# Kernel optimization log

Measured on AMD Instinct MI355X. Metric: run time of the kernel, lower is better.

Reference implementation:

```python
import jax, jax.numpy as jnp
import numpy as np

EPS = 1e-05


def layer_norm(x, a, b):
    m = jnp.mean(x, axis=-1, keepdims=True)
    v = jnp.var(x, axis=-1, keepdims=True)
    return a * (x - m) / jnp.sqrt(v + EPS) + b


def setup_inputs() -> dict:
    key = jax.random.key(0)
    ks = jax.random.split(key, 16)
    b, n, d, h = 1, 384, 128, 128
    s = 1.0 / np.sqrt(d)
    inp = {
        "x": jax.random.normal(ks[0], (b, n, n, d), dtype=jnp.float32),
        "norm_a": jnp.ones((d,), jnp.float32),
        "norm_b": jnp.zeros((d,), jnp.float32),
        "Wl": jax.random.normal(ks[1], (d, h), jnp.float32) * s,
        "bl": jnp.zeros((h,), jnp.float32),
        "Wr": jax.random.normal(ks[2], (d, h), jnp.float32) * s,
        "br": jnp.zeros((h,), jnp.float32),
        "Wlg": jax.random.normal(ks[3], (d, h), jnp.float32) * s,
        "blg": jnp.ones((h,), jnp.float32),
        "Wrg": jax.random.normal(ks[4], (d, h), jnp.float32) * s,
        "brg": jnp.ones((h,), jnp.float32),
        "Wog": jax.random.normal(ks[5], (d, h), jnp.float32) * s,
        "bog": jnp.ones((h,), jnp.float32),
        "on_a": jnp.ones((h,), jnp.float32),
        "on_b": jnp.zeros((h,), jnp.float32),
        "Wo": jax.random.normal(ks[6], (h, d), jnp.float32) * s,
        "bo": jnp.zeros((d,), jnp.float32),
    }
    return inp


def reference(x, norm_a, norm_b, Wl, bl, Wr, br, Wlg, blg, Wrg, brg, Wog, bog, on_a, on_b, Wo, bo):
    n = x.shape[1]
    xn = layer_norm(x, norm_a, norm_b)
    left = (xn @ Wl + bl) * jax.nn.sigmoid(xn @ Wlg + blg)
    right = (xn @ Wr + br) * jax.nn.sigmoid(xn @ Wrg + brg)
    out_gate = jax.nn.sigmoid(xn @ Wog + bog)
    # ingoing mix: out[b,i,j,d] = sum_k left[b,k,j,d] * right[b,k,i,d], in fp32
    out = jnp.einsum('bkjd,bkid->bijd', left.astype(jnp.float32), right.astype(jnp.float32)) / n
    out = out.astype(x.dtype)
    out = layer_norm(out, on_a, on_b) * out_gate
    return out @ Wo + bo
```

## Files before the change

kernel.cpp:

```cpp
#include <hip/hip_runtime.h>
#include <hip/hip_bf16.h>

#define NN 384
#define DD 128
#define MM (NN*NN)

typedef __attribute__((ext_vector_type(8))) short short8;
typedef __attribute__((ext_vector_type(4))) float f32x4;

__device__ __forceinline__ unsigned short f2bf(float f){
  unsigned u = __float_as_uint(f);
  u += 0x7fffu + ((u >> 16) & 1u);
  return (unsigned short)(u >> 16);
}
__device__ __forceinline__ float bf2f(unsigned short u){
  return __uint_as_float(((unsigned)u) << 16);
}
__device__ __forceinline__ float sigm(float x){
  return 1.0f / (1.0f + __expf(-x));
}
__device__ __forceinline__ unsigned cvtpk(float lo, float hi){
  unsigned r;
  asm("v_cvt_pk_bf16_f32 %0, %1, %2" : "=v"(r) : "v"(lo), "v"(hi));
  return r;
}
__device__ __forceinline__ f32x4 mfma16(short8 a, short8 b, f32x4 c){
  return __builtin_amdgcn_mfma_f32_16x16x32_bf16(a, b, c, 0, 0, 0);
}
__device__ __forceinline__ void gll16(const void* g, void* l){
  __builtin_amdgcn_global_load_lds(
      (const __attribute__((address_space(1))) unsigned int*)g,
      (__attribute__((address_space(3))) unsigned int*)l, 16, 0, 0);
}

__global__ void k_prep(const float* __restrict__ Wl, const float* __restrict__ Wlg,
                       const float* __restrict__ Wr, const float* __restrict__ Wrg,
                       const float* __restrict__ Wog, const float* __restrict__ Wo,
                       unsigned short* __restrict__ Wcat, unsigned short* __restrict__ Wot){
  int n = blockIdx.x;
  if(n < 640){
    const float* src; int col;
    if(n < 128){ src = Wl;  col = n; }
    else if(n < 256){ src = Wlg; col = n-128; }
    else if(n < 384){ src = Wr;  col = n-256; }
    else if(n < 512){ src = Wrg; col = n-384; }
    else            { src = Wog; col = n-512; }
    for(int k = threadIdx.x; k < 128; k += 64)
      Wcat[n*128 + k] = f2bf(src[k*128 + col]);
  } else {
    int c = n - 640;
    for(int k = threadIdx.x; k < 128; k += 64)
      Wot[c*128 + k] = f2bf(Wo[k*128 + c]);
  }
}

__global__ __launch_bounds__(256) void k_ln_x(const float* __restrict__ x,
    const float* __restrict__ na, const float* __restrict__ nb,
    unsigned short* __restrict__ xn){
  int wid = threadIdx.x >> 6, lane = threadIdx.x & 63;
  long r = (long)blockIdx.x*4 + wid;
  float2 v = *(const float2*)(x + r*DD + lane*2);
  float s  = v.x + v.y;
  float sq = v.x*v.x + v.y*v.y;
  #pragma unroll
  for(int m = 32; m >= 1; m >>= 1){ s += __shfl_xor(s, m); sq += __shfl_xor(sq, m); }
  float mean = s  * (1.0f/128.0f);
  float var  = sq * (1.0f/128.0f) - mean*mean;
  float rstd = rsqrtf(var + 1e-5f);
  float2 a = *(const float2*)(na + lane*2);
  float2 b = *(const float2*)(nb + lane*2);
  unsigned pk = (unsigned)f2bf(a.x*(v.x-mean)*rstd + b.x)
              | ((unsigned)f2bf(a.y*(v.y-mean)*rstd + b.y) << 16);
  *(unsigned*)(xn + r*DD + lane*2) = pk;
}

__global__ __launch_bounds__(256, 4) void k_proj(
    const unsigned short* __restrict__ xn, const unsigned short* __restrict__ Wcat,
    const float* __restrict__ bl, const float* __restrict__ blg,
    const float* __restrict__ br, const float* __restrict__ brg,
    unsigned short* __restrict__ Lt, unsigned short* __restrict__ Rt){
  __shared__ char lds[2][16384];
  const int tid = threadIdx.x;
  const int wid = tid >> 6, lane = tid & 63;
  const int lrow = lane & 15, lgrp = lane >> 4;
  const int b = blockIdx.x;
  const int f = b / 288;
  const int w = b % 288;

  const int ws = wid >> 1;
  const int wd = wid & 1;
  const int d  = f*32 + wd*16 + lrow;

  short8 bv[4], bg[4];
  #pragma unroll
  for(int ks = 0; ks < 4; ++ks){
    bv[ks] = *(const short8*)(Wcat + (ws*256 + d)*DD + ks*32 + lgrp*8);
    bg[ks] = *(const short8*)(Wcat + (ws*256 + 128 + d)*DD + ks*32 + lgrp*8);
  }
  const float b0v = (ws ? br  : bl )[d];
  const float b1v = (ws ? brg : blg)[d];
  const float sc  = ws ? 1.0f : (1.0f/384.0f);
  unsigned short* const base = (ws ? Rt : Lt) + (long)d*MM;

  auto stage = [&](int buf, int v){
    int j = v/6, kb = v%6;
    int rsub = lane >> 4, c = lane & 15;
    #pragma unroll
    for(int p = 0; p < 4; ++p){
      int r0 = p*16 + wid*4;
      int r = r0 + rsub;
      gll16(xn + ((long)(kb*64 + r)*NN + j)*DD + (c ^ (r & 7))*8, &lds[buf][r0*256]);
    }
  };

  stage(0, w*8);
  __syncthreads();
  int cur = 0;
  for(int i = 0; i < 8; ++i){
    int v = w*8 + i;
    if(i < 7) stage(cur^1, v+1);

    f32x4 zero = {0.f,0.f,0.f,0.f};
    f32x4 acc[4][2];
    #pragma unroll
    for(int a1=0;a1<4;++a1){ acc[a1][0] = zero; acc[a1][1] = zero; }

    #pragma unroll
    for(int ks = 0; ks < 4; ++ks){
      #pragma unroll
      for(int fr = 0; fr < 4; ++fr){
        int r = fr*16 + lrow;
        short8 af = *(const short8*)(&lds[cur][r*256 + (((ks*4+lgrp)*16) ^ ((r&7)<<4))]);
        acc[fr][0] = mfma16(af, bv[ks], acc[fr][0]);
        acc[fr][1] = mfma16(af, bg[ks], acc[fr][1]);
      }
    }

    int j = v/6, kb = v%6;
    unsigned short* dst = base + (long)j*NN + kb*64;
    #pragma unroll
    for(int fr = 0; fr < 4; ++fr){
      float v0 = (acc[fr][0][0] + b0v)*sigm(acc[fr][1][0] + b1v)*sc;
      float v1 = (acc[fr][0][1] + b0v)*sigm(acc[fr][1][1] + b1v)*sc;
      float v2 = (acc[fr][0][2] + b0v)*sigm(acc[fr][1][2] + b1v)*sc;
      float v3 = (acc[fr][0][3] + b0v)*sigm(acc[fr][1][3] + b1v)*sc;
      uint2 pk; pk.x = cvtpk(v0, v1); pk.y = cvtpk(v2, v3);
      *(uint2*)(dst + fr*16 + lgrp*4) = pk;
    }
    __syncthreads();
    cur ^= 1;
  }
}

__global__ __launch_bounds__(256) void k_einsum(
    const unsigned short* __restrict__ Rt, const unsigned short* __restrict__ Lt,
    unsigned short* __restrict__ mid){
  __shared__ char lds[65536];
  const int b = blockIdx.x;
  const int xcd = b & 7, slot = b >> 3;
  const int d = (slot/9)*8 + xcd;
  const int t = slot % 9;
  const int it = t/3, jt = t%3;
  const int i0 = it*128, j0 = jt*128;
  const unsigned short* Abase = Lt + (long)d*MM;
  const unsigned short* Bbase = Rt + (long)d*MM;
  const int wid = threadIdx.x >> 6, lane = threadIdx.x & 63;
  const int wr = wid >> 1, wc = wid & 1;
  const int lrow = lane & 15, lgrp = lane >> 4;

  auto stage = [&](int buf, int kt){
    int k = kt*64;
    int c = lane & 7;
    #pragma unroll
    for(int t8 = 0; t8 < 8; ++t8){
      int rr = wid*64 + t8*8 + (lane >> 3);
      int r = rr & 127;
      const unsigned short* src = (rr < 128) ? (Abase + (long)(j0+r)*NN + k)
                                             : (Bbase + (long)(i0+r)*NN + k);
      gll16(src + (c ^ (r & 7))*8, &lds[buf*32768 + (wid*64 + t8*8)*128]);
    }
  };

  f32x4 zero = {0.f,0.f,0.f,0.f};
  f32x4 acc[4][4];
  #pragma unroll
  for(int a1 = 0; a1 < 4; ++a1)
    #pragma unroll
    for(int a2 = 0; a2 < 4; ++a2) acc[a1][a2] = zero;

  stage(0, 0);
  __syncthreads();
  for(int kt = 0; kt < 6; ++kt){
    int cur = kt & 1;
    if(kt < 5) stage(cur ^ 1, kt + 1);
    const int base = cur*32768;
    #pragma unroll
    for(int ks = 0; ks < 2; ++ks){
      short8 af[4], bf[4];
      #pragma unroll
      for(int f = 0; f < 4; ++f){
        int rj = wr*64 + f*16 + lrow;
        af[f] = *(const short8*)(&lds[base + rj*128 + (((ks*4+lgrp)*16) ^ ((rj & 7) << 4))]);
        int ri = wc*64 + f*16 + lrow;
        bf[f] = *(const short8*)(&lds[base + 16384 + ri*128 + (((ks*4+lgrp)*16) ^ ((ri & 7) << 4))]);
      }
      #pragma unroll
      for(int fj = 0; fj < 4; ++fj)
        #pragma unroll
        for(int fi = 0; fi < 4; ++fi)
          acc[fj][fi] = mfma16(af[fj], bf[fi], acc[fj][fi]);
    }
    __syncthreads();
  }

  #pragma unroll
  for(int fj = 0; fj < 4; ++fj){
    int j = j0 + wr*64 + fj*16 + lgrp*4;
    #pragma unroll
    for(int fi = 0; fi < 4; ++fi){
      int i = i0 + wc*64 + fi*16 + lrow;
      uint2 pk;
      pk.x = cvtpk(acc[fj][fi][0], acc[fj][fi][1]);
      pk.y = cvtpk(acc[fj][fi][2], acc[fj][fi][3]);
      *(uint2*)(mid + (long)d*MM + (long)i*NN + j) = pk;
    }
  }
}

__global__ __launch_bounds__(256) void k_final(
    const unsigned short* __restrict__ mid, const unsigned short* __restrict__ xn,
    const unsigned short* __restrict__ Wcat,
    const float* __restrict__ bog,
    const float* __restrict__ ona, const float* __restrict__ onb,
    const unsigned short* __restrict__ Wot, const float* __restrict__ bo,
    float* __restrict__ out){
  __shared__ unsigned short midt[64][144];
  __shared__ char slds[16384];
  __shared__ char glds[16384];
  const int tid = threadIdx.x;
  const int wid = tid >> 6, lane = tid & 63;
  const int lrow = lane & 15, lgrp = lane >> 4;
  const int i = blockIdx.y;
  const int j0 = blockIdx.x*64;

  {
    int rsub = lane >> 4, c = lane & 15;
    #pragma unroll
    for(int p = 0; p < 4; ++p){
      int r0 = p*16 + wid*4;
      int r = r0 + rsub;
      gll16(xn + ((long)i*NN + j0 + r)*DD + (c ^ (r & 7))*8, &slds[r0*256]);
    }
  }
  const int wc = wid;
  short8 ag[2][4];
  #pragma unroll
  for(int cf = 0; cf < 2; ++cf)
    #pragma unroll
    for(int ks = 0; ks < 4; ++ks)
      ag[cf][ks] = *(const short8*)(Wcat + (512 + wc*32 + cf*16 + lrow)*DD + ks*32 + lgrp*8);

  {
    int jp = tid & 15, dr = tid >> 4;
    #pragma unroll
    for(int pass = 0; pass < 8; ++pass){
      int dd = pass*16 + dr;
      uint2 v = *(const uint2*)(mid + (long)dd*MM + (long)i*NN + j0 + jp*4);
      midt[jp*4+0][dd] = (unsigned short)(v.x & 0xffffu);
      midt[jp*4+1][dd] = (unsigned short)(v.x >> 16);
      midt[jp*4+2][dd] = (unsigned short)(v.y & 0xffffu);
      midt[jp*4+3][dd] = (unsigned short)(v.y >> 16);
    }
  }
  __syncthreads();

  {
    f32x4 zero = {0.f,0.f,0.f,0.f};
    f32x4 accg[2][4];
    #pragma unroll
    for(int a1=0;a1<2;++a1)
      #pragma unroll
      for(int a2=0;a2<4;++a2) accg[a1][a2] = zero;
    #pragma unroll
    for(int ks = 0; ks < 4; ++ks){
      short8 bx[4];
      #pragma unroll
      for(int mf = 0; mf < 4; ++mf){
        int r = mf*16 + lrow;
        bx[mf] = *(const short8*)(&slds[r*256 + (((ks*4+lgrp)*16) ^ ((r&7)<<4))]);
      }
      #pragma unroll
      for(int cf = 0; cf < 2; ++cf)
        #pragma unroll
        for(int mf = 0; mf < 4; ++mf)
          accg[cf][mf] = mfma16(ag[cf][ks], bx[mf], accg[cf][mf]);
    }
    #pragma unroll
    for(int cf = 0; cf < 2; ++cf){
      int c0 = wc*32 + cf*16 + lgrp*4;
      float4 b4 = *(const float4*)(bog + c0);
      #pragma unroll
      for(int mf = 0; mf < 4; ++mf){
        int rr = mf*16 + lrow;
        uint2 pk;
        pk.x = cvtpk(sigm(accg[cf][mf][0] + b4.x), sigm(accg[cf][mf][1] + b4.y));
        pk.y = cvtpk(sigm(accg[cf][mf][2] + b4.z), sigm(accg[cf][mf][3] + b4.w));
        *(uint2*)(&glds[rr*256 + ((c0*2) ^ ((rr&7)<<4))]) = pk;
      }
    }
  }
  __syncthreads();

  {
    int j = tid >> 2, s = tid & 3;
    float vals[32];
    float sum = 0.f, sq = 0.f;
    #pragma unroll
    for(int o8 = 0; o8 < 4; ++o8){
      short8 h = *(const short8*)(&midt[j][s*32 + o8*8]);
      #pragma unroll
      for(int q = 0; q < 8; ++q){
        float vq = bf2f((unsigned short)h[q]);
        vals[o8*8+q] = vq; sum += vq; sq += vq*vq;
      }
    }
    #pragma unroll
    for(int m = 1; m < 4; m <<= 1){ sum += __shfl_xor(sum, m); sq += __shfl_xor(sq, m); }
    float mean = sum*(1.f/128.f);
    float var  = sq *(1.f/128.f) - mean*mean;
    float rstd = rsqrtf(var + 1e-5f);
    #pragma unroll
    for(int o = 0; o < 32; o += 4){
      int dd = s*32 + o;
      uint2 gv = *(const uint2*)(&glds[j*256 + ((dd*2) ^ ((j&7)<<4))]);
      float g0 = bf2f((unsigned short)(gv.x & 0xffffu));
      float g1 = bf2f((unsigned short)(gv.x >> 16));
      float g2 = bf2f((unsigned short)(gv.y & 0xffffu));
      float g3 = bf2f((unsigned short)(gv.y >> 16));
      float4 a4 = *(const float4*)(ona + dd);
      float4 b4 = *(const float4*)(onb + dd);
      float v0 = (a4.x*(vals[o]  -mean)*rstd + b4.x)*g0;
      float v1 = (a4.y*(vals[o+1]-mean)*rstd + b4.y)*g1;
      float v2 = (a4.z*(vals[o+2]-mean)*rstd + b4.z)*g2;
      float v3 = (a4.w*(vals[o+3]-mean)*rstd + b4.w)*g3;
      uint2 pk; pk.x = cvtpk(v0, v1); pk.y = cvtpk(v2, v3);
      *(uint2*)(&slds[j*256 + ((dd*2) ^ ((j&7)<<4))]) = pk;
    }
  }
  __syncthreads();

  {
    f32x4 zero = {0.f,0.f,0.f,0.f};
    f32x4 acc[8];
    #pragma unroll
    for(int fc = 0; fc < 8; ++fc) acc[fc] = zero;
    #pragma unroll 1
    for(int ks = 0; ks < 4; ++ks){
      int row = wid*16 + lrow;
      short8 a = *(const short8*)(&slds[row*256 + (((ks*4+lgrp)*16) ^ ((row & 7) << 4))]);
      #pragma unroll
      for(int fc = 0; fc < 8; ++fc){
        int n = fc*16 + lrow;
        short8 bfr = *(const short8*)(Wot + n*DD + ks*32 + lgrp*8);
        acc[fc] = mfma16(a, bfr, acc[fc]);
      }
    }
    #pragma unroll
    for(int fc = 0; fc < 8; ++fc){
      int c = fc*16 + lrow;
      float bb = bo[c];
      #pragma unroll
      for(int q = 0; q < 4; ++q){
        int jl = wid*16 + lgrp*4 + q;
        out[((long)i*NN + j0 + jl)*DD + c] = acc[fc][q] + bb;
      }
    }
  }
}

extern "C" void kernel_launch(void* const* d_in, const int* in_sizes, int n_in,
                              void* d_out, int out_size, void* d_ws, size_t ws_size,
                              hipStream_t stream){
  const float* x   = (const float*)d_in[0];
  const float* na  = (const float*)d_in[1];
  const float* nb  = (const float*)d_in[2];
  const float* Wl  = (const float*)d_in[3];
  const float* bl  = (const float*)d_in[4];
  const float* Wr  = (const float*)d_in[5];
  const float* br  = (const float*)d_in[6];
  const float* Wlg = (const float*)d_in[7];
  const float* blg = (const float*)d_in[8];
  const float* Wrg = (const float*)d_in[9];
  const float* brg = (const float*)d_in[10];
  const float* Wog = (const float*)d_in[11];
  const float* bog = (const float*)d_in[12];
  const float* ona = (const float*)d_in[13];
  const float* onb = (const float*)d_in[14];
  const float* Wo  = (const float*)d_in[15];
  const float* bo  = (const float*)d_in[16];
  float* out = (float*)d_out;

  char* ws = (char*)d_ws;
  const size_t SZ = (size_t)MM*DD*2;
  unsigned short* xn   = (unsigned short*)(ws);
  unsigned short* Lt   = (unsigned short*)(ws + SZ);
  unsigned short* Rt   = (unsigned short*)(ws + 2*SZ);
  unsigned short* mid  = (unsigned short*)(ws + 3*SZ);
  unsigned short* Wcat = (unsigned short*)(ws + 4*SZ);
  unsigned short* Wot  = (unsigned short*)(ws + 4*SZ + (size_t)640*128*2);

  k_prep  <<<768, 64, 0, stream>>>(Wl, Wlg, Wr, Wrg, Wog, Wo, Wcat, Wot);
  k_ln_x  <<<MM/4, 256, 0, stream>>>(x, na, nb, xn);
  k_proj  <<<1152, 256, 0, stream>>>(xn, Wcat, bl, blg, br, brg, Lt, Rt);
  k_einsum<<<1152, 256, 0, stream>>>(Rt, Lt, mid);
  k_final <<<dim3(6, 384), 256, 0, stream>>>(mid, xn, Wcat, bog, ona, onb, Wot, bo, out);
}
```

Measured before the change: 197.2 us.

## Reuse one LDS buffer for gate and output, preload Wo fragments, vectorize stores

```diff
diff --git a/kernel.cpp b/kernel.cpp
--- a/kernel.cpp
+++ b/kernel.cpp
@@ -234,14 +234,14 @@
     const float* __restrict__ ona, const float* __restrict__ onb,
     const unsigned short* __restrict__ Wot, const float* __restrict__ bo,
     float* __restrict__ out){
-  __shared__ unsigned short midt[64][144];
+  __shared__ unsigned short midt[64][136];
   __shared__ char slds[16384];
-  __shared__ char glds[16384];
   const int tid = threadIdx.x;
   const int wid = tid >> 6, lane = tid & 63;
   const int lrow = lane & 15, lgrp = lane >> 4;
   const int i = blockIdx.y;
   const int j0 = blockIdx.x*64;
+  const int wc = wid;
 
   {
     int rsub = lane >> 4, c = lane & 15;
@@ -252,7 +252,6 @@
       gll16(xn + ((long)i*NN + j0 + r)*DD + (c ^ (r & 7))*8, &slds[r0*256]);
     }
   }
-  const int wc = wid;
   short8 ag[2][4];
   #pragma unroll
   for(int cf = 0; cf < 2; ++cf)
@@ -274,27 +273,37 @@
   }
   __syncthreads();
 
+  f32x4 zero = {0.f,0.f,0.f,0.f};
+  f32x4 accg[2][4];
+  #pragma unroll
+  for(int a1=0;a1<2;++a1)
+    #pragma unroll
+    for(int a2=0;a2<4;++a2) accg[a1][a2] = zero;
+  #pragma unroll
+  for(int ks = 0; ks < 4; ++ks){
+    short8 bx[4];
+    #pragma unroll
+    for(int mf = 0; mf < 4; ++mf){
+      int r = mf*16 + lrow;
+      bx[mf] = *(const short8*)(&slds[r*256 + (((ks*4+lgrp)*16) ^ ((r&7)<<4))]);
+    }
+    #pragma unroll
+    for(int cf = 0; cf < 2; ++cf)
+      #pragma unroll
+      for(int mf = 0; mf < 4; ++mf)
+        accg[cf][mf] = mfma16(ag[cf][ks], bx[mf], accg[cf][mf]);
+  }
+
+  short8 aw[2][4];
+  #pragma unroll
+  for(int cf = 0; cf < 2; ++cf)
+    #pragma unroll
+    for(int ks = 0; ks < 4; ++ks)
+      aw[cf][ks] = *(const short8*)(Wot + (wc*32 + cf*16 + lrow)*DD + ks*32 + lgrp*8);
+
+  __syncthreads();
+
   {
-    f32x4 zero = {0.f,0.f,0.f,0.f};
-    f32x4 accg[2][4];
-    #pragma unroll
-    for(int a1=0;a1<2;++a1)
-      #pragma unroll
-      for(int a2=0;a2<4;++a2) accg[a1][a2] = zero;
-    #pragma unroll
-    for(int ks = 0; ks < 4; ++ks){
-      short8 bx[4];
-      #pragma unroll
-      for(int mf = 0; mf < 4; ++mf){
-        int r = mf*16 + lrow;
-        bx[mf] = *(const short8*)(&slds[r*256 + (((ks*4+lgrp)*16) ^ ((r&7)<<4))]);
-      }
-      #pragma unroll
-      for(int cf = 0; cf < 2; ++cf)
-        #pragma unroll
-        for(int mf = 0; mf < 4; ++mf)
-          accg[cf][mf] = mfma16(ag[cf][ks], bx[mf], accg[cf][mf]);
-    }
     #pragma unroll
     for(int cf = 0; cf < 2; ++cf){
       int c0 = wc*32 + cf*16 + lgrp*4;
@@ -305,7 +314,7 @@
         uint2 pk;
         pk.x = cvtpk(sigm(accg[cf][mf][0] + b4.x), sigm(accg[cf][mf][1] + b4.y));
         pk.y = cvtpk(sigm(accg[cf][mf][2] + b4.z), sigm(accg[cf][mf][3] + b4.w));
-        *(uint2*)(&glds[rr*256 + ((c0*2) ^ ((rr&7)<<4))]) = pk;
+        *(uint2*)(&slds[rr*256 + ((c0*2) ^ ((rr&7)<<4))]) = pk;
       }
     }
   }
@@ -332,7 +341,8 @@
     #pragma unroll
     for(int o = 0; o < 32; o += 4){
       int dd = s*32 + o;
-      uint2 gv = *(const uint2*)(&glds[j*256 + ((dd*2) ^ ((j&7)<<4))]);
+      char* gp = &slds[j*256 + ((dd*2) ^ ((j&7)<<4))];
+      uint2 gv = *(uint2*)gp;
       float g0 = bf2f((unsigned short)(gv.x & 0xffffu));
       float g1 = bf2f((unsigned short)(gv.x >> 16));
       float g2 = bf2f((unsigned short)(gv.y & 0xffffu));
@@ -344,35 +354,44 @@
       float v2 = (a4.z*(vals[o+2]-mean)*rstd + b4.z)*g2;
       float v3 = (a4.w*(vals[o+3]-mean)*rstd + b4.w)*g3;
       uint2 pk; pk.x = cvtpk(v0, v1); pk.y = cvtpk(v2, v3);
-      *(uint2*)(&slds[j*256 + ((dd*2) ^ ((j&7)<<4))]) = pk;
+      *(uint2*)gp = pk;
     }
   }
   __syncthreads();
 
   {
-    f32x4 zero = {0.f,0.f,0.f,0.f};
-    f32x4 acc[8];
-    #pragma unroll
-    for(int fc = 0; fc < 8; ++fc) acc[fc] = zero;
-    #pragma unroll 1
+    f32x4 acco[2][4];
+    #pragma unroll
+    for(int a1=0;a1<2;++a1)
+      #pragma unroll
+      for(int a2=0;a2<4;++a2) acco[a1][a2] = zero;
+    #pragma unroll
     for(int ks = 0; ks < 4; ++ks){
-      int row = wid*16 + lrow;
-      short8 a = *(const short8*)(&slds[row*256 + (((ks*4+lgrp)*16) ^ ((row & 7) << 4))]);
-      #pragma unroll
-      for(int fc = 0; fc < 8; ++fc){
-        int n = fc*16 + lrow;
-        short8 bfr = *(const short8*)(Wot + n*DD + ks*32 + lgrp*8);
-        acc[fc] = mfma16(a, bfr, acc[fc]);
-      }
-    }
-    #pragma unroll
-    for(int fc = 0; fc < 8; ++fc){
-      int c = fc*16 + lrow;
-      float bb = bo[c];
-      #pragma unroll
-      for(int q = 0; q < 4; ++q){
-        int jl = wid*16 + lgrp*4 + q;
-        out[((long)i*NN + j0 + jl)*DD + c] = acc[fc][q] + bb;
+      short8 bx[4];
+      #pragma unroll
+      for(int mf = 0; mf < 4; ++mf){
+        int r = mf*16 + lrow;
+        bx[mf] = *(const short8*)(&slds[r*256 + (((ks*4+lgrp)*16) ^ ((r&7)<<4))]);
+      }
+      #pragma unroll
+      for(int cf = 0; cf < 2; ++cf)
+        #pragma unroll
+        for(int mf = 0; mf < 4; ++mf)
+          acco[cf][mf] = mfma16(aw[cf][ks], bx[mf], acco[cf][mf]);
+    }
+    #pragma unroll
+    for(int cf = 0; cf < 2; ++cf){
+      int c0 = wc*32 + cf*16 + lgrp*4;
+      float4 b4 = *(const float4*)(bo + c0);
+      #pragma unroll
+      for(int mf = 0; mf < 4; ++mf){
+        int jl = mf*16 + lrow;
+        float4 v;
+        v.x = acco[cf][mf][0] + b4.x;
+        v.y = acco[cf][mf][1] + b4.y;
+        v.z = acco[cf][mf][2] + b4.z;
+        v.w = acco[cf][mf][3] + b4.w;
+        *(float4*)(out + ((long)i*NN + j0 + jl)*DD + c0) = v;
       }
     }
   }
```

New measurement: 180.1 us. -8.6%, faster.

## Make final kernel persistent over three tiles with double-buffered xn and mid prefetch

Applied to the files above, without the earlier changes.

```diff
diff --git a/kernel.cpp b/kernel.cpp
--- a/kernel.cpp
+++ b/kernel.cpp
@@ -227,155 +227,193 @@
   }
 }
 
-__global__ __launch_bounds__(256) void k_final(
+__global__ __launch_bounds__(256, 3) void k_final(
     const unsigned short* __restrict__ mid, const unsigned short* __restrict__ xn,
     const unsigned short* __restrict__ Wcat,
     const float* __restrict__ bog,
     const float* __restrict__ ona, const float* __restrict__ onb,
     const unsigned short* __restrict__ Wot, const float* __restrict__ bo,
     float* __restrict__ out){
-  __shared__ unsigned short midt[64][144];
-  __shared__ char slds[16384];
-  __shared__ char glds[16384];
+  __shared__ char Xb[2][16384];
+  __shared__ unsigned short midt[64][136];
+  __shared__ float clds[512];
   const int tid = threadIdx.x;
   const int wid = tid >> 6, lane = tid & 63;
   const int lrow = lane & 15, lgrp = lane >> 4;
-  const int i = blockIdx.y;
-  const int j0 = blockIdx.x*64;
-
-  {
-    int rsub = lane >> 4, c = lane & 15;
-    #pragma unroll
-    for(int p = 0; p < 4; ++p){
-      int r0 = p*16 + wid*4;
-      int r = r0 + rsub;
-      gll16(xn + ((long)i*NN + j0 + r)*DD + (c ^ (r & 7))*8, &slds[r0*256]);
-    }
-  }
-  const int wc = wid;
-  short8 ag[2][4];
+  const int jp = tid & 15, dr = tid >> 4;
+  const int u0 = blockIdx.x * 3;
+
+  uint2 mA[8], mB[8];
+
+#define STAGE_XN(buf, uu) {                                                   \
+    int i_ = (uu)/6, jj_ = ((uu)%6)*64;                                       \
+    int rsub = lane >> 4, cc = lane & 15;                                     \
+    _Pragma("unroll")                                                         \
+    for(int p = 0; p < 4; ++p){                                               \
+      int r0 = p*16 + wid*4;                                                  \
+      int r = r0 + rsub;                                                      \
+      gll16(xn + ((long)i_*NN + jj_ + r)*DD + (cc ^ (r & 7))*8,               \
+            &Xb[buf][r0*256]);                                                \
+    } }
+
+#define LOAD_MID(reg, uu) {                                                   \
+    int i_ = (uu)/6, jj_ = ((uu)%6)*64;                                       \
+    const unsigned short* mp = mid + (long)i_*NN + jj_ + jp*4;                \
+    _Pragma("unroll")                                                         \
+    for(int p = 0; p < 8; ++p)                                                \
+      reg[p] = *(const uint2*)(mp + (long)(p*16 + dr)*MM);                    \
+  }
+
+#define WRITE_MIDT(reg) {                                                     \
+    _Pragma("unroll")                                                         \
+    for(int p = 0; p < 8; ++p){                                               \
+      int dd = p*16 + dr;                                                     \
+      midt[jp*4+0][dd] = (unsigned short)(reg[p].x & 0xffffu);                \
+      midt[jp*4+1][dd] = (unsigned short)(reg[p].x >> 16);                    \
+      midt[jp*4+2][dd] = (unsigned short)(reg[p].y & 0xffffu);                \
+      midt[jp*4+3][dd] = (unsigned short)(reg[p].y >> 16);                    \
+    } }
+
+  short8 ag[2][4], aw[2][4];
   #pragma unroll
   for(int cf = 0; cf < 2; ++cf)
     #pragma unroll
-    for(int ks = 0; ks < 4; ++ks)
-      ag[cf][ks] = *(const short8*)(Wcat + (512 + wc*32 + cf*16 + lrow)*DD + ks*32 + lgrp*8);
-
-  {
-    int jp = tid & 15, dr = tid >> 4;
-    #pragma unroll
-    for(int pass = 0; pass < 8; ++pass){
-      int dd = pass*16 + dr;
-      uint2 v = *(const uint2*)(mid + (long)dd*MM + (long)i*NN + j0 + jp*4);
-      midt[jp*4+0][dd] = (unsigned short)(v.x & 0xffffu);
-      midt[jp*4+1][dd] = (unsigned short)(v.x >> 16);
-      midt[jp*4+2][dd] = (unsigned short)(v.y & 0xffffu);
-      midt[jp*4+3][dd] = (unsigned short)(v.y >> 16);
-    }
-  }
+    for(int ks = 0; ks < 4; ++ks){
+      ag[cf][ks] = *(const short8*)(Wcat + (512 + wid*32 + cf*16 + lrow)*DD + ks*32 + lgrp*8);
+      aw[cf][ks] = *(const short8*)(Wot  + (      wid*32 + cf*16 + lrow)*DD + ks*32 + lgrp*8);
+    }
+  if(tid < 128){
+    clds[tid]       = ona[tid];
+    clds[128 + tid] = onb[tid];
+    clds[256 + tid] = bog[tid];
+    clds[384 + tid] = bo[tid];
+  }
+
+  STAGE_XN(0, u0);
+  LOAD_MID(mA, u0);
   __syncthreads();
 
-  {
-    f32x4 zero = {0.f,0.f,0.f,0.f};
-    f32x4 accg[2][4];
-    #pragma unroll
-    for(int a1=0;a1<2;++a1)
-      #pragma unroll
-      for(int a2=0;a2<4;++a2) accg[a1][a2] = zero;
-    #pragma unroll
-    for(int ks = 0; ks < 4; ++ks){
-      short8 bx[4];
-      #pragma unroll
-      for(int mf = 0; mf < 4; ++mf){
-        int r = mf*16 + lrow;
-        bx[mf] = *(const short8*)(&slds[r*256 + (((ks*4+lgrp)*16) ^ ((r&7)<<4))]);
-      }
-      #pragma unroll
-      for(int cf = 0; cf < 2; ++cf)
-        #pragma unroll
-        for(int mf = 0; mf < 4; ++mf)
-          accg[cf][mf] = mfma16(ag[cf][ks], bx[mf], accg[cf][mf]);
-    }
-    #pragma unroll
-    for(int cf = 0; cf < 2; ++cf){
-      int c0 = wc*32 + cf*16 + lgrp*4;
-      float4 b4 = *(const float4*)(bog + c0);
-      #pragma unroll
-      for(int mf = 0; mf < 4; ++mf){
-        int rr = mf*16 + lrow;
-        uint2 pk;
-        pk.x = cvtpk(sigm(accg[cf][mf][0] + b4.x), sigm(accg[cf][mf][1] + b4.y));
-        pk.y = cvtpk(sigm(accg[cf][mf][2] + b4.z), sigm(accg[cf][mf][3] + b4.w));
-        *(uint2*)(&glds[rr*256 + ((c0*2) ^ ((rr&7)<<4))]) = pk;
-      }
-    }
-  }
-  __syncthreads();
-
-  {
-    int j = tid >> 2, s = tid & 3;
-    float vals[32];
-    float sum = 0.f, sq = 0.f;
-    #pragma unroll
-    for(int o8 = 0; o8 < 4; ++o8){
-      short8 h = *(const short8*)(&midt[j][s*32 + o8*8]);
-      #pragma unroll
-      for(int q = 0; q < 8; ++q){
-        float vq = bf2f((unsigned short)h[q]);
-        vals[o8*8+q] = vq; sum += vq; sq += vq*vq;
-      }
-    }
-    #pragma unroll
-    for(int m = 1; m < 4; m <<= 1){ sum += __shfl_xor(sum, m); sq += __shfl_xor(sq, m); }
-    float mean = sum*(1.f/128.f);
-    float var  = sq *(1.f/128.f) - mean*mean;
-    float rstd = rsqrtf(var + 1e-5f);
-    #pragma unroll
-    for(int o = 0; o < 32; o += 4){
-      int dd = s*32 + o;
-      uint2 gv = *(const uint2*)(&glds[j*256 + ((dd*2) ^ ((j&7)<<4))]);
-      float g0 = bf2f((unsigned short)(gv.x & 0xffffu));
-      float g1 = bf2f((unsigned short)(gv.x >> 16));
-      float g2 = bf2f((unsigned short)(gv.y & 0xffffu));
-      float g3 = bf2f((unsigned short)(gv.y >> 16));
-      float4 a4 = *(const float4*)(ona + dd);
-      float4 b4 = *(const float4*)(onb + dd);
-      float v0 = (a4.x*(vals[o]  -mean)*rstd + b4.x)*g0;
-      float v1 = (a4.y*(vals[o+1]-mean)*rstd + b4.y)*g1;
-      float v2 = (a4.z*(vals[o+2]-mean)*rstd + b4.z)*g2;
-      float v3 = (a4.w*(vals[o+3]-mean)*rstd + b4.w)*g3;
-      uint2 pk; pk.x = cvtpk(v0, v1); pk.y = cvtpk(v2, v3);
-      *(uint2*)(&slds[j*256 + ((dd*2) ^ ((j&7)<<4))]) = pk;
-    }
-  }
-  __syncthreads();
-
-  {
-    f32x4 zero = {0.f,0.f,0.f,0.f};
-    f32x4 acc[8];
-    #pragma unroll
-    for(int fc = 0; fc < 8; ++fc) acc[fc] = zero;
-    #pragma unroll 1
-    for(int ks = 0; ks < 4; ++ks){
-      int row = wid*16 + lrow;
-      short8 a = *(const short8*)(&slds[row*256 + (((ks*4+lgrp)*16) ^ ((row & 7) << 4))]);
-      #pragma unroll
-      for(int fc = 0; fc < 8; ++fc){
-        int n = fc*16 + lrow;
-        short8 bfr = *(const short8*)(Wot + n*DD + ks*32 + lgrp*8);
-        acc[fc] = mfma16(a, bfr, acc[fc]);
-      }
-    }
-    #pragma unroll
-    for(int fc = 0; fc < 8; ++fc){
-      int c = fc*16 + lrow;
-      float bb = bo[c];
-      #pragma unroll
-      for(int q = 0; q < 4; ++q){
-        int jl = wid*16 + lgrp*4 + q;
-        out[((long)i*NN + j0 + jl)*DD + c] = acc[fc][q] + bb;
-      }
-    }
-  }
+#define UNIT(T, MREG, MNXT, CUR) {                                            \
+    const int u_ = u0 + (T);                                                  \
+    const int iU = u_/6, jU = (u_%6)*64;                                      \
+    if((T) < 2){ STAGE_XN((CUR)^1, u_+1); LOAD_MID(MNXT, u_+1); }             \
+    WRITE_MIDT(MREG);                                                         \
+    f32x4 zero_ = {0.f,0.f,0.f,0.f};                                          \
+    f32x4 accg[2][4];                                                         \
+    _Pragma("unroll")                                                         \
+    for(int a1=0;a1<2;++a1){ _Pragma("unroll")                                \
+      for(int a2=0;a2<4;++a2) accg[a1][a2] = zero_; }                         \
+    _Pragma("unroll")                                                         \
+    for(int ks = 0; ks < 4; ++ks){                                            \
+      short8 bx[4];                                                           \
+      _Pragma("unroll")                                                       \
+      for(int mf = 0; mf < 4; ++mf){                                          \
+        int r = mf*16 + lrow;                                                 \
+        bx[mf] = *(const short8*)(&Xb[CUR][r*256 + (((ks*4+lgrp)*16) ^ ((r&7)<<4))]); \
+      }                                                                       \
+      _Pragma("unroll")                                                       \
+      for(int cf = 0; cf < 2; ++cf){ _Pragma("unroll")                        \
+        for(int mf = 0; mf < 4; ++mf)                                         \
+          accg[cf][mf] = mfma16(ag[cf][ks], bx[mf], accg[cf][mf]); }          \
+    }                                                                         \
+    __syncthreads();   \
+    _Pragma("unroll")                                                         \
+    for(int cf = 0; cf < 2; ++cf){                                            \
+      int c0 = wid*32 + cf*16 + lgrp*4;                                       \
+      float4 g4 = *(const float4*)&clds[256 + c0];                            \
+      _Pragma("unroll")                                                       \
+      for(int mf = 0; mf < 4; ++mf){                                          \
+        int rr = mf*16 + lrow;                                                \
+        uint2 pk;                                                             \
+        pk.x = cvtpk(sigm(accg[cf][mf][0]+g4.x), sigm(accg[cf][mf][1]+g4.y)); \
+        pk.y = cvtpk(sigm(accg[cf][mf][2]+g4.z), sigm(accg[cf][mf][3]+g4.w)); \
+        *(uint2*)(&Xb[CUR][rr*256 + ((c0*2) ^ ((rr&7)<<4))]) = pk;            \
+      }                                                                       \
+    }                                                                         \
+    __syncthreads();                                      \
+    {                                                                         \
+      int j_ = tid >> 2, s_ = tid & 3;                                        \
+      float sum = 0.f, sq = 0.f;                                              \
+      _Pragma("unroll")                                                       \
+      for(int o8 = 0; o8 < 4; ++o8){                                          \
+        short8 h = *(const short8*)(&midt[j_][s_*32 + o8*8]);                 \
+        _Pragma("unroll")                                                     \
+        for(int q = 0; q < 8; ++q){                                           \
+          float vq = bf2f((unsigned short)h[q]);                              \
+          sum += vq; sq += vq*vq;                                             \
+        }                                                                     \
+      }                                                                       \
+      sum += __shfl_xor(sum,1); sq += __shfl_xor(sq,1);                       \
+      sum += __shfl_xor(sum,2); sq += __shfl_xor(sq,2);                       \
+      float mean = sum*(1.f/128.f);                                           \
+      float var  = sq *(1.f/128.f) - mean*mean;                               \
+      float rstd = rsqrtf(var + 1e-5f);                                       \
+      _Pragma("unroll")                                                       \
+      for(int o = 0; o < 32; o += 4){                                         \
+        int dd = s_*32 + o;                                                   \
+        char* gp = &Xb[CUR][j_*256 + ((dd*2) ^ ((j_&7)<<4))];                 \
+        uint2 gv = *(uint2*)gp;                                               \
+        uint2 mv = *(const uint2*)(&midt[j_][dd]);                            \
+        float m0 = bf2f((unsigned short)(mv.x & 0xffffu));                    \
+        float m1 = bf2f((unsigned short)(mv.x >> 16));                        \
+        float m2 = bf2f((unsigned short)(mv.y & 0xffffu));                    \
+        float m3 = bf2f((unsigned short)(mv.y >> 16));                        \
+        float4 a4 = *(const float4*)&clds[dd];                                \
+        float4 b4 = *(const float4*)&clds[128 + dd];                          \
+        float v0 = (a4.x*(m0-mean)*rstd + b4.x)*bf2f((unsigned short)(gv.x & 0xffffu)); \
+        float v1 = (a4.y*(m1-mean)*rstd + b4.y)*bf2f((unsigned short)(gv.x >> 16));     \
+        float v2 = (a4.z*(m2-mean)*rstd + b4.z)*bf2f((unsigned short)(gv.y & 0xffffu)); \
+        float v3 = (a4.w*(m3-mean)*rstd + b4.w)*bf2f((unsigned short)(gv.y >> 16));     \
+        uint2 pk; pk.x = cvtpk(v0, v1); pk.y = cvtpk(v2, v3);                 \
+        *(uint2*)gp = pk;                                                     \
+      }                                                                       \
+    }                                                                         \
+    __syncthreads();                                       \
+    {                                                                         \
+      f32x4 acco[2][4];                                                       \
+      _Pragma("unroll")                                                       \
+      for(int a1=0;a1<2;++a1){ _Pragma("unroll")                              \
+        for(int a2=0;a2<4;++a2) acco[a1][a2] = zero_; }                       \
+      _Pragma("unroll")                                                       \
+      for(int ks = 0; ks < 4; ++ks){                                          \
+        short8 bx[4];                                                         \
+        _Pragma("unroll")                                                     \
+        for(int mf = 0; mf < 4; ++mf){                                        \
+          int r = mf*16 + lrow;                                               \
+          bx[mf] = *(const short8*)(&Xb[CUR][r*256 + (((ks*4+lgrp)*16) ^ ((r&7)<<4))]); \
+        }                                                                     \
+        _Pragma("unroll")                                                     \
+        for(int cf = 0; cf < 2; ++cf){ _Pragma("unroll")                      \
+          for(int mf = 0; mf < 4; ++mf)                                       \
+            acco[cf][mf] = mfma16(aw[cf][ks], bx[mf], acco[cf][mf]); }        \
+      }                                                                       \
+      _Pragma("unroll")                                                       \
+      for(int cf = 0; cf < 2; ++cf){                                          \
+        int c0 = wid*32 + cf*16 + lgrp*4;                                     \
+        float4 b4 = *(const float4*)&clds[384 + c0];                          \
+        _Pragma("unroll")                                                     \
+        for(int mf = 0; mf < 4; ++mf){                                        \
+          int jl = mf*16 + lrow;                                              \
+          float4 v;                                                           \
+          v.x = acco[cf][mf][0] + b4.x;                                       \
+          v.y = acco[cf][mf][1] + b4.y;                                       \
+          v.z = acco[cf][mf][2] + b4.z;                                       \
+          v.w = acco[cf][mf][3] + b4.w;                                       \
+          *(float4*)(out + ((long)iU*NN + jU + jl)*DD + c0) = v;              \
+        }                                                                     \
+      }                                                                       \
+    }                                                                         \
+    __syncthreads();  \
+  }
+
+  UNIT(0, mA, mB, 0)
+  UNIT(1, mB, mA, 1)
+  UNIT(2, mA, mB, 0)
+
+#undef UNIT
+#undef STAGE_XN
+#undef LOAD_MID
+#undef WRITE_MIDT
 }
 
 extern "C" void kernel_launch(void* const* d_in, const int* in_sizes, int n_in,
@@ -413,5 +451,5 @@
   k_ln_x  <<<MM/4, 256, 0, stream>>>(x, na, nb, xn);
   k_proj  <<<1152, 256, 0, stream>>>(xn, Wcat, bl, blg, br, brg, Lt, Rt);
   k_einsum<<<1152, 256, 0, stream>>>(Rt, Lt, mid);
-  k_final <<<dim3(6, 384), 256, 0, stream>>>(mid, xn, Wcat, bog, ona, onb, Wot, bo, out);
-}
+  k_final <<<768, 256, 0, stream>>>(mid, xn, Wcat, bog, ona, onb, Wot, bo, out);
+}
```

Measured after the change: 166.7 us. 15.4% less time.

## Restructure final kernel: two tiles per block with register prefetch and reduced LDS

Applied to the files above, without the earlier changes.

```diff
diff --git a/kernel.cpp b/kernel.cpp
--- a/kernel.cpp
+++ b/kernel.cpp
@@ -31,6 +31,10 @@
   __builtin_amdgcn_global_load_lds(
       (const __attribute__((address_space(1))) unsigned int*)g,
       (__attribute__((address_space(3))) unsigned int*)l, 16, 0, 0);
+}
+__device__ __forceinline__ void barL(){
+  asm volatile("s_waitcnt lgkmcnt(0)" ::: "memory");
+  __builtin_amdgcn_s_barrier();
 }
 
 __global__ void k_prep(const float* __restrict__ Wl, const float* __restrict__ Wlg,
@@ -227,155 +231,210 @@
   }
 }
 
-__global__ __launch_bounds__(256) void k_final(
+__global__ __launch_bounds__(256, 4) void k_final(
     const unsigned short* __restrict__ mid, const unsigned short* __restrict__ xn,
     const unsigned short* __restrict__ Wcat,
     const float* __restrict__ bog,
     const float* __restrict__ ona, const float* __restrict__ onb,
     const unsigned short* __restrict__ Wot, const float* __restrict__ bo,
     float* __restrict__ out){
-  __shared__ unsigned short midt[64][144];
-  __shared__ char slds[16384];
-  __shared__ char glds[16384];
+  __shared__ char Xb[16384];
+  __shared__ float4 wavep[128];
+  __shared__ float2 statB[64];
+  __shared__ float clds[512];
   const int tid = threadIdx.x;
   const int wid = tid >> 6, lane = tid & 63;
   const int lrow = lane & 15, lgrp = lane >> 4;
-  const int i = blockIdx.y;
-  const int j0 = blockIdx.x*64;
-
-  {
-    int rsub = lane >> 4, c = lane & 15;
-    #pragma unroll
-    for(int p = 0; p < 4; ++p){
-      int r0 = p*16 + wid*4;
-      int r = r0 + rsub;
-      gll16(xn + ((long)i*NN + j0 + r)*DD + (c ^ (r & 7))*8, &slds[r0*256]);
-    }
-  }
-  const int wc = wid;
-  short8 ag[2][4];
-  #pragma unroll
-  for(int cf = 0; cf < 2; ++cf)
-    #pragma unroll
-    for(int ks = 0; ks < 4; ++ks)
-      ag[cf][ks] = *(const short8*)(Wcat + (512 + wc*32 + cf*16 + lrow)*DD + ks*32 + lgrp*8);
-
-  {
-    int jp = tid & 15, dr = tid >> 4;
-    #pragma unroll
-    for(int pass = 0; pass < 8; ++pass){
-      int dd = pass*16 + dr;
-      uint2 v = *(const uint2*)(mid + (long)dd*MM + (long)i*NN + j0 + jp*4);
-      midt[jp*4+0][dd] = (unsigned short)(v.x & 0xffffu);
-      midt[jp*4+1][dd] = (unsigned short)(v.x >> 16);
-      midt[jp*4+2][dd] = (unsigned short)(v.y & 0xffffu);
-      midt[jp*4+3][dd] = (unsigned short)(v.y >> 16);
-    }
-  }
+  const int jp = tid & 15, dr = tid >> 4;
+  const int xr = tid >> 2, xq = tid & 3;
+
+  const int u0 = blockIdx.x * 2;
+
+  short8 xnA[4], xnB[4];
+  uint2  mA[8], mB[8];
+
+  auto ldxn = [&](short8 (&r)[4], int u){
+    int i_ = u/6; long base = ((long)i_*NN + (u%6)*64 + xr)*DD;
+    #pragma unroll
+    for(int p = 0; p < 4; ++p)
+      r[p] = *(const short8*)(xn + base + (p*4 + xq)*8);
+  };
+  auto ldmid = [&](uint2 (&r)[8], int u){
+    int i_ = u/6; long base = (long)i_*NN + (u%6)*64 + jp*4;
+    #pragma unroll
+    for(int p = 0; p < 8; ++p)
+      r[p] = *(const uint2*)(mid + (long)(dr*8 + p)*MM + base);
+  };
+  auto wrxn = [&](short8 (&r)[4]){
+    #pragma unroll
+    for(int p = 0; p < 4; ++p)
+      *(short8*)(&Xb[xr*256 + (((p*4 + xq)*16) ^ ((xr & 7) << 4))]) = r[p];
+  };
+
+  ldxn(xnA, u0);
+  ldmid(mA, u0);
+  if(tid < 128){
+    clds[tid]       = ona[tid];
+    clds[128 + tid] = onb[tid];
+    clds[256 + tid] = bog[tid];
+    clds[384 + tid] = bo[tid];
+  }
+  wrxn(xnA);
   __syncthreads();
 
-  {
-    f32x4 zero = {0.f,0.f,0.f,0.f};
+  auto unit = [&](int u, uint2 (&mc)[8], short8 (&xnn)[4], uint2 (&mn)[8],
+                  bool hasNext){
+    const int iU = u/6, jU = (u%6)*64;
+
+    if(hasNext){ ldxn(xnn, u+1); ldmid(mn, u+1); }
+
     f32x4 accg[2][4];
     #pragma unroll
-    for(int a1=0;a1<2;++a1)
-      #pragma unroll
-      for(int a2=0;a2<4;++a2) accg[a1][a2] = zero;
+    for(int cf = 0; cf < 2; ++cf){
+      int c0 = wid*32 + cf*16 + lgrp*4;
+      float4 b4 = *(const float4*)&clds[256 + c0];
+      #pragma unroll
+      for(int mf = 0; mf < 4; ++mf) accg[cf][mf] = (f32x4){b4.x, b4.y, b4.z, b4.w};
+    }
     #pragma unroll
     for(int ks = 0; ks < 4; ++ks){
+      short8 ag[2];
+      #pragma unroll
+      for(int cf = 0; cf < 2; ++cf)
+        ag[cf] = *(const short8*)(Wcat + (512 + wid*32 + cf*16 + lrow)*DD + ks*32 + lgrp*8);
       short8 bx[4];
       #pragma unroll
       for(int mf = 0; mf < 4; ++mf){
         int r = mf*16 + lrow;
-        bx[mf] = *(const short8*)(&slds[r*256 + (((ks*4+lgrp)*16) ^ ((r&7)<<4))]);
+        bx[mf] = *(const short8*)(&Xb[r*256 + (((ks*4+lgrp)*16) ^ ((r&7)<<4))]);
       }
       #pragma unroll
       for(int cf = 0; cf < 2; ++cf)
         #pragma unroll
         for(int mf = 0; mf < 4; ++mf)
-          accg[cf][mf] = mfma16(ag[cf][ks], bx[mf], accg[cf][mf]);
-    }
+          accg[cf][mf] = mfma16(ag[cf], bx[mf], accg[cf][mf]);
+    }
+    {
+      float s0=0,s1=0,s2=0,s3=0, q0=0,q1=0,q2=0,q3=0;
+      #pragma unroll
+      for(int p = 0; p < 8; ++p){
+        float v0 = bf2f((unsigned short)(mc[p].x & 0xffffu));
+        float v1 = bf2f((unsigned short)(mc[p].x >> 16));
+        float v2 = bf2f((unsigned short)(mc[p].y & 0xffffu));
+        float v3 = bf2f((unsigned short)(mc[p].y >> 16));
+        s0 += v0; q0 += v0*v0;  s1 += v1; q1 += v1*v1;
+        s2 += v2; q2 += v2*v2;  s3 += v3; q3 += v3*v3;
+      }
+      #pragma unroll
+      for(int m = 16; m <= 32; m <<= 1){
+        s0 += __shfl_xor(s0,m); q0 += __shfl_xor(q0,m);
+        s1 += __shfl_xor(s1,m); q1 += __shfl_xor(q1,m);
+        s2 += __shfl_xor(s2,m); q2 += __shfl_xor(q2,m);
+        s3 += __shfl_xor(s3,m); q3 += __shfl_xor(q3,m);
+      }
+      if(lane < 16){
+        wavep[(wid*16 + lane)*2 + 0] = (float4){s0, q0, s1, q1};
+        wavep[(wid*16 + lane)*2 + 1] = (float4){s2, q2, s3, q3};
+      }
+    }
+    barL();
+
     #pragma unroll
     for(int cf = 0; cf < 2; ++cf){
-      int c0 = wc*32 + cf*16 + lgrp*4;
-      float4 b4 = *(const float4*)(bog + c0);
+      int c0 = wid*32 + cf*16 + lgrp*4;
       #pragma unroll
       for(int mf = 0; mf < 4; ++mf){
-        int rr = mf*16 + lrow;
+        int j = mf*16 + lrow;
         uint2 pk;
-        pk.x = cvtpk(sigm(accg[cf][mf][0] + b4.x), sigm(accg[cf][mf][1] + b4.y));
-        pk.y = cvtpk(sigm(accg[cf][mf][2] + b4.z), sigm(accg[cf][mf][3] + b4.w));
-        *(uint2*)(&glds[rr*256 + ((c0*2) ^ ((rr&7)<<4))]) = pk;
-      }
-    }
-  }
-  __syncthreads();
-
-  {
-    int j = tid >> 2, s = tid & 3;
-    float vals[32];
-    float sum = 0.f, sq = 0.f;
-    #pragma unroll
-    for(int o8 = 0; o8 < 4; ++o8){
-      short8 h = *(const short8*)(&midt[j][s*32 + o8*8]);
-      #pragma unroll
-      for(int q = 0; q < 8; ++q){
-        float vq = bf2f((unsigned short)h[q]);
-        vals[o8*8+q] = vq; sum += vq; sq += vq*vq;
-      }
-    }
-    #pragma unroll
-    for(int m = 1; m < 4; m <<= 1){ sum += __shfl_xor(sum, m); sq += __shfl_xor(sq, m); }
-    float mean = sum*(1.f/128.f);
-    float var  = sq *(1.f/128.f) - mean*mean;
-    float rstd = rsqrtf(var + 1e-5f);
-    #pragma unroll
-    for(int o = 0; o < 32; o += 4){
-      int dd = s*32 + o;
-      uint2 gv = *(const uint2*)(&glds[j*256 + ((dd*2) ^ ((j&7)<<4))]);
-      float g0 = bf2f((unsigned short)(gv.x & 0xffffu));
-      float g1 = bf2f((unsigned short)(gv.x >> 16));
-      float g2 = bf2f((unsigned short)(gv.y & 0xffffu));
-      float g3 = bf2f((unsigned short)(gv.y >> 16));
-      float4 a4 = *(const float4*)(ona + dd);
-      float4 b4 = *(const float4*)(onb + dd);
-      float v0 = (a4.x*(vals[o]  -mean)*rstd + b4.x)*g0;
-      float v1 = (a4.y*(vals[o+1]-mean)*rstd + b4.y)*g1;
-      float v2 = (a4.z*(vals[o+2]-mean)*rstd + b4.z)*g2;
-      float v3 = (a4.w*(vals[o+3]-mean)*rstd + b4.w)*g3;
-      uint2 pk; pk.x = cvtpk(v0, v1); pk.y = cvtpk(v2, v3);
-      *(uint2*)(&slds[j*256 + ((dd*2) ^ ((j&7)<<4))]) = pk;
-    }
-  }
-  __syncthreads();
-
-  {
-    f32x4 zero = {0.f,0.f,0.f,0.f};
-    f32x4 acc[8];
-    #pragma unroll
-    for(int fc = 0; fc < 8; ++fc) acc[fc] = zero;
-    #pragma unroll 1
-    for(int ks = 0; ks < 4; ++ks){
-      int row = wid*16 + lrow;
-      short8 a = *(const short8*)(&slds[row*256 + (((ks*4+lgrp)*16) ^ ((row & 7) << 4))]);
+        pk.x = cvtpk(sigm(accg[cf][mf][0]), sigm(accg[cf][mf][1]));
+        pk.y = cvtpk(sigm(accg[cf][mf][2]), sigm(accg[cf][mf][3]));
+        *(uint2*)(&Xb[j*256 + ((c0*2) ^ ((j&7)<<4))]) = pk;
+      }
+    }
+    if(tid < 64){
+      int jpp = tid >> 2, jjj = tid & 3;
+      float s = 0.f, q = 0.f;
+      #pragma unroll
+      for(int w = 0; w < 4; ++w){
+        float4 f = wavep[(w*16 + jpp)*2 + (jjj >> 1)];
+        if(jjj & 1){ s += f.z; q += f.w; } else { s += f.x; q += f.y; }
+      }
+      float mean = s*(1.f/128.f);
+      float var  = q*(1.f/128.f) - mean*mean;
+      statB[tid] = (float2){mean, rsqrtf(var + 1e-5f)};
+    }
+    barL();
+
+    {
+      float4 a0 = *(const float4*)&clds[dr*8];
+      float4 a1 = *(const float4*)&clds[dr*8 + 4];
+      float4 b0 = *(const float4*)&clds[128 + dr*8];
+      float4 b1 = *(const float4*)&clds[128 + dr*8 + 4];
+      float av[8] = {a0.x,a0.y,a0.z,a0.w,a1.x,a1.y,a1.z,a1.w};
+      float bv[8] = {b0.x,b0.y,b0.z,b0.w,b1.x,b1.y,b1.z,b1.w};
+      #pragma unroll
+      for(int jj = 0; jj < 4; ++jj){
+        int j = jp*4 + jj;
+        float2 mr = statB[j];
+        char* gp = &Xb[j*256 + ((dr*16) ^ ((j&7)<<4))];
+        short8 g8 = *(const short8*)gp;
+        float vv[8];
+        #pragma unroll
+        for(int p = 0; p < 8; ++p){
+          unsigned w = (jj & 1) ? ((jj & 2) ? (mc[p].y >> 16) : (mc[p].x >> 16))
+                                : ((jj & 2) ? (mc[p].y & 0xffffu) : (mc[p].x & 0xffffu));
+          float m = bf2f((unsigned short)w);
+          float g = bf2f((unsigned short)g8[p]);
+          vv[p] = (av[p]*(m - mr.x)*mr.y + bv[p]) * g;
+        }
+        short8 o;
+        #pragma unroll
+        for(int p = 0; p < 4; ++p){
+          unsigned pk = cvtpk(vv[p*2], vv[p*2+1]);
+          o[p*2] = (short)(pk & 0xffffu); o[p*2+1] = (short)(pk >> 16);
+        }
+        *(short8*)gp = o;
+      }
+    }
+    barL();
+
+    {
+      f32x4 acc[8];
       #pragma unroll
       for(int fc = 0; fc < 8; ++fc){
-        int n = fc*16 + lrow;
-        short8 bfr = *(const short8*)(Wot + n*DD + ks*32 + lgrp*8);
-        acc[fc] = mfma16(a, bfr, acc[fc]);
-      }
-    }
-    #pragma unroll
-    for(int fc = 0; fc < 8; ++fc){
-      int c = fc*16 + lrow;
-      float bb = bo[c];
-      #pragma unroll
-      for(int q = 0; q < 4; ++q){
-        int jl = wid*16 + lgrp*4 + q;
-        out[((long)i*NN + j0 + jl)*DD + c] = acc[fc][q] + bb;
-      }
-    }
-  }
+        float bb = clds[384 + fc*16 + lrow];
+        acc[fc] = (f32x4){bb, bb, bb, bb};
+      }
+      #pragma unroll
+      for(int ks = 0; ks < 4; ++ks){
+        int r = wid*16 + lrow;
+        short8 af = *(const short8*)(&Xb[r*256 + (((ks*4+lgrp)*16) ^ ((r&7)<<4))]);
+        #pragma unroll
+        for(int fc = 0; fc < 8; ++fc){
+          short8 bw = *(const short8*)(Wot + (fc*16 + lrow)*DD + ks*32 + lgrp*8);
+          acc[fc] = mfma16(af, bw, acc[fc]);
+        }
+      }
+      #pragma unroll
+      for(int fc = 0; fc < 8; ++fc){
+        int c = fc*16 + lrow;
+        #pragma unroll
+        for(int q = 0; q < 4; ++q){
+          int jl = wid*16 + lgrp*4 + q;
+          out[((long)iU*NN + jU + jl)*DD + c] = acc[fc][q];
+        }
+      }
+    }
+    barL();
+
+    if(hasNext){
+      wrxn(xnn);
+      barL();
+    }
+  };
+
+  unit(u0,     mA, xnB, mB, true);
+  unit(u0 + 1, mB, xnA, mA, false);
 }
 
 extern "C" void kernel_launch(void* const* d_in, const int* in_sizes, int n_in,
@@ -413,5 +472,5 @@
   k_ln_x  <<<MM/4, 256, 0, stream>>>(x, na, nb, xn);
   k_proj  <<<1152, 256, 0, stream>>>(xn, Wcat, bl, blg, br, brg, Lt, Rt);
   k_einsum<<<1152, 256, 0, stream>>>(Rt, Lt, mid);
-  k_final <<<dim3(6, 384), 256, 0, stream>>>(mid, xn, Wcat, bog, ona, onb, Wot, bo, out);
-}
+  k_final <<<1152, 256, 0, stream>>>(mid, xn, Wcat, bog, ona, onb, Wot, bo, out);
+}
```

Result: slower. 276.3 us (+40.2%).
